# Optimization experiments

Hardware: AMD Instinct MI355X
Metric: run time of the kernel (lower is better)

The kernel has to match this reference:

```python
import jax, jax.numpy as jnp
import numpy as np

HID = 2048
NH = 16
HD = HID // NH  # 128
THETA = 10000.0


def _rope_cos_sin(position_ids):
    # inv_freq: [HD/2]
    inv_freq = 1.0 / (THETA ** (jnp.arange(0, HD, 2, dtype=jnp.float32) / HD))
    freqs = position_ids.astype(jnp.float32)[:, :, None] * inv_freq[None, None, :]  # [b,s,hd/2]
    emb = jnp.concatenate([freqs, freqs], axis=-1)  # [b,s,hd]
    return jnp.cos(emb), jnp.sin(emb)


def _rotate_half(x):
    x1, x2 = x[..., : HD // 2], x[..., HD // 2:]
    return jnp.concatenate([-x2, x1], axis=-1)


def setup_inputs() -> dict:
    key = jax.random.key(0)
    ks = jax.random.split(key, 10)
    b, s = 2, 2048
    scale = 1.0 / np.sqrt(HID)
    hidden_states = jax.random.normal(ks[0], (b, s, HID), dtype=jnp.float32)
    wq = jax.random.normal(ks[1], (HID, HID), dtype=jnp.float32) * scale
    wk = jax.random.normal(ks[2], (HID, HID), dtype=jnp.float32) * scale
    wv = jax.random.normal(ks[3], (HID, HID), dtype=jnp.float32) * scale
    wo = jax.random.normal(ks[4], (HID, HID), dtype=jnp.float32) * scale
    bq = jnp.zeros((HID,), jnp.float32)
    bk = jnp.zeros((HID,), jnp.float32)
    bv = jnp.zeros((HID,), jnp.float32)
    bo = jnp.zeros((HID,), jnp.float32)
    # HF-style additive causal mask [b,1,q,kv]: 0 on/below diag, large negative above
    neg = jnp.finfo(jnp.float32).min
    causal = jnp.where(jnp.tril(jnp.ones((s, s), dtype=bool)), 0.0, neg)
    attention_mask = jnp.broadcast_to(causal[None, None], (b, 1, s, s)).astype(jnp.float32)
    position_ids = jnp.broadcast_to(jnp.arange(s, dtype=jnp.int32)[None], (b, s))
    return {
        "hidden_states": hidden_states,
        "wq": wq, "bq": bq, "wk": wk, "bk": bk,
        "wv": wv, "bv": bv, "wo": wo, "bo": bo,
        "attention_mask": attention_mask, "position_ids": position_ids,
    }


def reference(hidden_states, wq, bq, wk, bk, wv, bv, wo, bo, attention_mask, position_ids):
    b, s, _ = hidden_states.shape
    q = hidden_states @ wq.T + bq  # [b,s,hid]
    k = hidden_states @ wk.T + bk
    v = hidden_states @ wv.T + bv
    # [b, nh, s, hd]
    q = q.reshape(b, s, NH, HD).transpose(0, 2, 1, 3)
    k = k.reshape(b, s, NH, HD).transpose(0, 2, 1, 3)
    v = v.reshape(b, s, NH, HD).transpose(0, 2, 1, 3)
    cos, sin = _rope_cos_sin(position_ids)  # [b,s,hd]
    cos, sin = cos[:, None], sin[:, None]  # unsqueeze_dim=1 -> [b,1,s,hd]
    q = q * cos + _rotate_half(q) * sin
    k = k * cos + _rotate_half(k) * sin
    scores = jnp.einsum("bhqd,bhkd->bhqk", q, k) / np.sqrt(HD)
    scores = scores + attention_mask
    attn = jax.nn.softmax(scores.astype(jnp.float32), axis=-1).astype(q.dtype)
    out = jnp.einsum("bhqk,bhkd->bhqd", attn, v)  # [b,nh,s,hd]
    out = out.transpose(0, 2, 1, 3).reshape(b, s, HID)
    return out @ wo.T + bo
```

## Files before the change

kernel.cpp:

```cpp
#include <hip/hip_runtime.h>

#define S_LEN 2048
#define HID   2048
#define NHEAD 16
#define HDIM  128
#define BATCH 2
#define KDIM  2048

using bf16x8  = __attribute__((ext_vector_type(8))) short;
using f32x4   = __attribute__((ext_vector_type(4))) float;
using f32x16  = __attribute__((ext_vector_type(16))) float;
using short4v = __attribute__((ext_vector_type(4))) short;
using uint4v  = __attribute__((ext_vector_type(4))) unsigned;

__device__ __forceinline__ short f2bf(float f) {
  union { float f; unsigned u; } v; v.f = f;
  unsigned r = v.u + 0x7fffu + ((v.u >> 16) & 1u);
  return (short)(r >> 16);
}
__device__ __forceinline__ float bf2f(short s) {
  union { unsigned u; float f; } v;
  v.u = ((unsigned)(unsigned short)s) << 16;
  return v.f;
}

__device__ __forceinline__ void gl_lds16(const void* g, void* l) {
  __builtin_amdgcn_global_load_lds(
      (const __attribute__((address_space(1))) void*)g,
      (__attribute__((address_space(3))) void*)l, 16, 0, 0);
}

__global__ __launch_bounds__(256)
void convert_all(const float* __restrict__ hs, const float* __restrict__ wq,
                 const float* __restrict__ wk, const float* __restrict__ wv,
                 const float* __restrict__ wo,
                 short* __restrict__ hsb, short* __restrict__ wqkv,
                 short* __restrict__ wob)
{
  const int base = blockIdx.x * 256 + threadIdx.x;
#pragma unroll
  for (int it = 0; it < 6; ++it) {
    int j = base + it * 524288;
    const float* src; short* dst;
    if (j < 1048576)      { src = hs; dst = hsb; }
    else if (j < 1572864) { j -= 1048576; src = wq; dst = wqkv; }
    else if (j < 2097152) { j -= 1572864; src = wk; dst = wqkv + 4194304; }
    else if (j < 2621440) { j -= 2097152; src = wv; dst = wqkv + 8388608; }
    else                  { j -= 2621440; src = wo; dst = wob; }
    f32x4 a = ((const f32x4*)src)[2 * j];
    f32x4 b = ((const f32x4*)src)[2 * j + 1];
    bf16x8 o;
    o[0]=f2bf(a[0]); o[1]=f2bf(a[1]); o[2]=f2bf(a[2]); o[3]=f2bf(a[3]);
    o[4]=f2bf(b[0]); o[5]=f2bf(b[1]); o[6]=f2bf(b[2]); o[7]=f2bf(b[3]);
    ((bf16x8*)dst)[j] = o;
  }
}

template<int KIND>
__global__ __launch_bounds__(256)
void gemm128(const short* __restrict__ A, const short* __restrict__ B,
             const float* __restrict__ bias0, const float* __restrict__ bias1,
             const float* __restrict__ bias2,
             void* __restrict__ O0, void* __restrict__ O1, void* __restrict__ O2)
{
  __shared__ __align__(16) short As[128 * 64];
  __shared__ __align__(16) short Bs[128 * 64];
  const int tid  = threadIdx.x;
  const int lane = tid & 63, wave = tid >> 6;
  const int ln = lane & 15, g = lane >> 4;
  const int wr = wave >> 1, wc = wave & 1;
  const int m0 = blockIdx.x * 128, n0 = blockIdx.y * 128;

  const int srow   = tid >> 3;
  const int schunk = (tid & 7) ^ (srow & 7);
  const short* aS = A + (size_t)(m0 + srow) * KDIM + schunk * 8;
  const short* bS = B + (size_t)(n0 + srow) * KDIM + schunk * 8;

  f32x4 acc[4][4] = {};

  for (int k0 = 0; k0 < KDIM; k0 += 64) {
    __syncthreads();
#pragma unroll
    for (int j = 0; j < 4; ++j) {
      gl_lds16(aS + k0 + j * (32 * KDIM), &As[j * 2048 + tid * 8]);
      gl_lds16(bS + k0 + j * (32 * KDIM), &Bs[j * 2048 + tid * 8]);
    }
    __syncthreads();

#pragma unroll
    for (int ks = 0; ks < 2; ++ks) {
      bf16x8 af[4], bfm[4];
#pragma unroll
      for (int i = 0; i < 4; ++i) {
        const int r = wr * 64 + i * 16 + ln;
        af[i] = *(const bf16x8*)&As[r * 64 + (((ks * 4 + g) ^ (r & 7)) << 3)];
      }
#pragma unroll
      for (int j2 = 0; j2 < 4; ++j2) {
        const int r = wc * 64 + j2 * 16 + ln;
        bfm[j2] = *(const bf16x8*)&Bs[r * 64 + (((ks * 4 + g) ^ (r & 7)) << 3)];
      }
#pragma unroll
      for (int i = 0; i < 4; ++i)
#pragma unroll
        for (int j2 = 0; j2 < 4; ++j2)
          acc[i][j2] = __builtin_amdgcn_mfma_f32_16x16x32_bf16(af[i], bfm[j2], acc[i][j2], 0, 0, 0);
    }
  }

  if constexpr (KIND == 0) {
    const int seg   = n0 >> 11;
    const int nbase = (n0 & 2047) + wc * 64;
    const float* bias = (seg == 0) ? bias0 : (seg == 1) ? bias1 : bias2;
    float bvv[4];
#pragma unroll
    for (int j = 0; j < 4; ++j) bvv[j] = bias[nbase + j * 16 + ln];
    if (seg < 2) {
      short* C = (short*)(seg ? O1 : O0);
#pragma unroll
      for (int i = 0; i < 4; ++i) {
        const int mb = m0 + wr * 64 + i * 16 + 4 * g;
#pragma unroll
        for (int j = 0; j < 4; ++j) {
          const int nl = nbase + j * 16 + ln;
          const int h = nl >> 7, d = nl & 127;
#pragma unroll
          for (int e = 0; e < 4; ++e) {
            const int m = mb + e, bb = m >> 11, t = m & (S_LEN - 1);
            C[((size_t)((bb * NHEAD + h) * S_LEN + t) << 7) + d] = f2bf(acc[i][j][e] + bvv[j]);
          }
        }
      }
    } else {
      short* C = (short*)O2;
#pragma unroll
      for (int i = 0; i < 4; ++i) {
        const int mb = m0 + wr * 64 + i * 16 + 4 * g;
        const int bb = mb >> 11, t0 = mb & (S_LEN - 1);
#pragma unroll
        for (int j = 0; j < 4; ++j) {
          const int nl = nbase + j * 16 + ln;
          const int h = nl >> 7, d = nl & 127;
          short4v v;
#pragma unroll
          for (int e = 0; e < 4; ++e) v[e] = f2bf(acc[i][j][e] + bvv[j]);
          *(short4v*)&C[((size_t)((bb * NHEAD + h) * HDIM + d)) * S_LEN + t0] = v;
        }
      }
    }
  } else {
    float* C = (float*)O0;
    float bvv[4];
#pragma unroll
    for (int j = 0; j < 4; ++j) bvv[j] = bias0[n0 + wc * 64 + j * 16 + ln];
#pragma unroll
    for (int i = 0; i < 4; ++i) {
      const int mb = m0 + wr * 64 + i * 16 + 4 * g;
#pragma unroll
      for (int j = 0; j < 4; ++j) {
        const int n = n0 + wc * 64 + j * 16 + ln;
#pragma unroll
        for (int e = 0; e < 4; ++e)
          C[(size_t)(mb + e) * HID + n] = acc[i][j][e] + bvv[j];
      }
    }
  }
}

#define QSCALE 0.12752767502f
__global__ __launch_bounds__(256)
void rope_kernel(short* __restrict__ Qb, short* __restrict__ Kb,
                 const int* __restrict__ pos_ids)
{
  const int row = blockIdx.x * 4 + (threadIdx.x >> 6);
  const int d   = threadIdx.x & 63;
  const int bh  = row >> 11, t = row & (S_LEN - 1);
  const int b   = bh >> 4;
  const float pos = (float)pos_ids[b * S_LEN + t];
  const float inv = exp2f((float)d * -0.20762050593f);
  float s, c;
  sincosf(pos * inv, &s, &c);
  const size_t base = (size_t)row * HDIM;
  {
    float x1 = bf2f(Qb[base + d]), x2 = bf2f(Qb[base + d + 64]);
    Qb[base + d]      = f2bf((x1 * c - x2 * s) * QSCALE);
    Qb[base + d + 64] = f2bf((x2 * c + x1 * s) * QSCALE);
  }
  {
    float x1 = bf2f(Kb[base + d]), x2 = bf2f(Kb[base + d + 64]);
    Kb[base + d]      = f2bf(x1 * c - x2 * s);
    Kb[base + d + 64] = f2bf(x2 * c + x1 * s);
  }
}

__global__ __launch_bounds__(256)
void attn_kernel(const short* __restrict__ Qb, const short* __restrict__ Kb,
                 const short* __restrict__ Vt, short* __restrict__ AO)
{
  __shared__ __align__(16) short Ks[128 * 128];
  __shared__ __align__(16) short Vs[128 * 128];
  const int tid  = threadIdx.x;
  const int wave = tid >> 6, lane = tid & 63;
  const int lq = lane & 31, lh = lane >> 5;
  const int bid = blockIdx.x;
  const int bh  = bid & 31;
  const int grp = bid >> 5;
  const int yt  = (grp & 7) ^ ((grp & 8) ? 15 : 0);
  const int qw  = yt * 128 + wave * 32;
  const int q   = qw + lq;

  const short* Kbh = Kb + (size_t)bh * (S_LEN * HDIM);
  const short* Vbh = Vt + (size_t)bh * (S_LEN * HDIM);
  const int sw   = ((tid & 15) ^ ((tid >> 4) & 7)) << 3;
  const int kOff = (tid >> 4) * HDIM + sw;
  const int vOff = (tid >> 4) * S_LEN + sw;

  bf16x8 qf[8];
#pragma unroll
  for (int kk = 0; kk < 8; ++kk)
    qf[kk] = *(const bf16x8*)&Qb[((size_t)bh * S_LEN + q) * HDIM + kk * 16 + lh * 8];

  f32x16 o[4] = {};
  float m_s = -3.0e38f, l_s = 0.f;

  for (int kvt = 0; kvt <= yt; ++kvt) {
    const int kv0 = kvt * 128;
    __syncthreads();
#pragma unroll
    for (int p = 0; p < 8; ++p) {
      gl_lds16(Kbh + (size_t)kv0 * HDIM + kOff + p * (16 * HDIM), &Ks[p * 2048 + tid * 8]);
      gl_lds16(Vbh + kv0 + vOff + p * (16 * S_LEN),               &Vs[p * 2048 + tid * 8]);
    }
    __syncthreads();

#pragma unroll
    for (int h = 0; h < 2; ++h) {
      f32x16 sfr[2] = {};
      __builtin_amdgcn_s_setprio(1);
#pragma unroll
      for (int kk = 0; kk < 8; ++kk) {
#pragma unroll
        for (int nt = 0; nt < 2; ++nt) {
          const int row = h * 64 + nt * 32 + lq;
          bf16x8 ak = *(const bf16x8*)&Ks[(row * 128 + kk * 16 + lh * 8) ^ ((row & 7) << 3)];
          sfr[nt] = __builtin_amdgcn_mfma_f32_32x32x16_bf16(ak, qf[kk], sfr[nt], 0, 0, 0);
        }
      }
      __builtin_amdgcn_s_setprio(0);

      if (kvt == yt) {
#pragma unroll
        for (int nt = 0; nt < 2; ++nt) {
          const int kvb = kv0 + h * 64 + nt * 32 + 4 * lh;
#pragma unroll
          for (int r = 0; r < 16; ++r) {
            const int kv = kvb + (r & 3) + 8 * (r >> 2);
            if (kv > q) sfr[nt][r] = -3.0e38f;
          }
        }
      }
      float rmax = -3.0e38f;
#pragma unroll
      for (int nt = 0; nt < 2; ++nt)
#pragma unroll
        for (int r = 0; r < 16; ++r) rmax = fmaxf(rmax, sfr[nt][r]);
      rmax = fmaxf(rmax, __shfl_xor(rmax, 32));

      if (__any(rmax > m_s + 8.0f)) {
        const float nm = fmaxf(m_s, rmax);
        const float corr = exp2f(m_s - nm);
        m_s = nm;
        l_s *= corr;
#pragma unroll
        for (int dt = 0; dt < 4; ++dt)
#pragma unroll
          for (int r = 0; r < 16; ++r) o[dt][r] *= corr;
      }

      float ps = 0.f;
#pragma unroll
      for (int nt = 0; nt < 2; ++nt)
#pragma unroll
        for (int r = 0; r < 16; ++r) {
          const float pv = exp2f(sfr[nt][r] - m_s);
          sfr[nt][r] = pv;
          ps += pv;
        }
      l_s += ps;

      bf16x8 pa[4];
#pragma unroll
      for (int kk = 0; kk < 4; ++kk) {
        const int nt = kk >> 1, c8 = (kk & 1) * 8;
        unsigned w0, w1, w2, w3;
        asm("v_cvt_pk_bf16_f32 %0, %1, %2" : "=v"(w0) : "v"(sfr[nt][c8 + 0]), "v"(sfr[nt][c8 + 1]));
        asm("v_cvt_pk_bf16_f32 %0, %1, %2" : "=v"(w1) : "v"(sfr[nt][c8 + 2]), "v"(sfr[nt][c8 + 3]));
        asm("v_cvt_pk_bf16_f32 %0, %1, %2" : "=v"(w2) : "v"(sfr[nt][c8 + 4]), "v"(sfr[nt][c8 + 5]));
        asm("v_cvt_pk_bf16_f32 %0, %1, %2" : "=v"(w3) : "v"(sfr[nt][c8 + 6]), "v"(sfr[nt][c8 + 7]));
        asm volatile("v_permlane32_swap_b32 %0, %1" : "+v"(w0), "+v"(w2));
        asm volatile("v_permlane32_swap_b32 %0, %1" : "+v"(w1), "+v"(w3));
        uint4v u; u[0] = w0; u[1] = w1; u[2] = w2; u[3] = w3;
        pa[kk] = __builtin_bit_cast(bf16x8, u);
      }

      __builtin_amdgcn_s_setprio(1);
#pragma unroll
      for (int kk = 0; kk < 4; ++kk) {
#pragma unroll
        for (int dt = 0; dt < 4; ++dt) {
          const int row = dt * 32 + lq;
          bf16x8 av = *(const bf16x8*)&Vs[(row * 128 + h * 64 + kk * 16 + lh * 8) ^ ((row & 7) << 3)];
          o[dt] = __builtin_amdgcn_mfma_f32_32x32x16_bf16(av, pa[kk], o[dt], 0, 0, 0);
        }
      }
      __builtin_amdgcn_s_setprio(0);
    }
  }

  l_s += __shfl_xor(l_s, 32);
  const float inv = 1.0f / l_s;
  const int b = bh >> 4, hh = bh & 15;
  short* dst = &AO[((size_t)b * S_LEN + q) * HID + hh * HDIM];
#pragma unroll
  for (int dt = 0; dt < 4; ++dt) {
#pragma unroll
    for (int rq = 0; rq < 4; ++rq) {
      short4v v4;
#pragma unroll
      for (int e = 0; e < 4; ++e) v4[e] = f2bf(o[dt][rq * 4 + e] * inv);
      *(short4v*)&dst[dt * 32 + rq * 8 + 4 * lh] = v4;
    }
  }
}

extern "C" void kernel_launch(void* const* d_in, const int* in_sizes, int n_in,
                              void* d_out, int out_size, void* d_ws, size_t ws_size,
                              hipStream_t stream)
{
  const float* hs = (const float*)d_in[0];
  const float* wq = (const float*)d_in[1];
  const float* bq = (const float*)d_in[2];
  const float* wk = (const float*)d_in[3];
  const float* bk = (const float*)d_in[4];
  const float* wv = (const float*)d_in[5];
  const float* bv = (const float*)d_in[6];
  const float* wo = (const float*)d_in[7];
  const float* bo = (const float*)d_in[8];
  const int*  pos = (const int*)d_in[10];
  float* out = (float*)d_out;

  const size_t TSZ = (size_t)BATCH * NHEAD * S_LEN * HDIM;
  short* Qb   = (short*)d_ws;
  short* Kb   = Qb + TSZ;
  short* Vt   = Kb + TSZ;
  short* hsb  = Vt + TSZ;
  short* AO   = hsb;
  short* Wqkv = hsb + TSZ;
  short* wob  = Wqkv + 12582912;

  convert_all<<<2048, 256, 0, stream>>>(hs, wq, wk, wv, wo, hsb, Wqkv, wob);
  gemm128<0><<<dim3(32, 48), 256, 0, stream>>>(hsb, Wqkv, bq, bk, bv, Qb, Kb, Vt);
  rope_kernel<<<(BATCH * NHEAD * S_LEN) / 4, 256, 0, stream>>>(Qb, Kb, pos);
  attn_kernel<<<512, 256, 0, stream>>>(Qb, Kb, Vt, AO);
  gemm128<1><<<dim3(32, 16), 256, 0, stream>>>(AO, wob, bo, nullptr, nullptr, out, nullptr, nullptr);
}
```

Measured before the change: 254.3 us.

## Use 128x256 GEMM tiles with triple-buffered async LDS pipeline

Replaces the 128x128, 256-thread GEMM with a 128x256 tile computed by 512 threads. K-tiles are triple-buffered in LDS with loads issued two tiles ahead and partial vmcnt waits. Global loads are interleaved between MFMA phases, with setprio raised around the MFMA blocks. The goal is to hide global-to-LDS latency and raise MFMA utilisation in the QKV and output projections. The cost is more LDS per block (about 144KB) and fewer blocks in the grid, which may limit occupancy and wave-level parallelism.

```diff
diff --git a/kernel.cpp b/kernel.cpp
--- a/kernel.cpp
+++ b/kernel.cpp
@@ -57,93 +57,125 @@
 }
 
 template<int KIND>
-__global__ __launch_bounds__(256)
-void gemm128(const short* __restrict__ A, const short* __restrict__ B,
+__global__ __launch_bounds__(512)
+void gemm256(const short* __restrict__ A, const short* __restrict__ B,
              const float* __restrict__ bias0, const float* __restrict__ bias1,
              const float* __restrict__ bias2,
              void* __restrict__ O0, void* __restrict__ O1, void* __restrict__ O2)
 {
-  __shared__ __align__(16) short As[128 * 64];
-  __shared__ __align__(16) short Bs[128 * 64];
+  __shared__ __align__(16) short LA[3 * 8192];
+  __shared__ __align__(16) short LB[3 * 16384];
   const int tid  = threadIdx.x;
   const int lane = tid & 63, wave = tid >> 6;
   const int ln = lane & 15, g = lane >> 4;
-  const int wr = wave >> 1, wc = wave & 1;
-  const int m0 = blockIdx.x * 128, n0 = blockIdx.y * 128;
+  const int wm = wave >> 2, wn = wave & 3;
+  const int m0 = blockIdx.x * 128, n0 = blockIdx.y * 256;
 
   const int srow   = tid >> 3;
   const int schunk = (tid & 7) ^ (srow & 7);
   const short* aS = A + (size_t)(m0 + srow) * KDIM + schunk * 8;
   const short* bS = B + (size_t)(n0 + srow) * KDIM + schunk * 8;
 
+  const int rA = wm * 64 + ln;
+  const int rB = wn * 64 + ln;
+  const int axor = rA & 7, bxor = rB & 7;
+
   f32x4 acc[4][4] = {};
 
-  for (int k0 = 0; k0 < KDIM; k0 += 64) {
-    __syncthreads();
-#pragma unroll
-    for (int j = 0; j < 4; ++j) {
-      gl_lds16(aS + k0 + j * (32 * KDIM), &As[j * 2048 + tid * 8]);
-      gl_lds16(bS + k0 + j * (32 * KDIM), &Bs[j * 2048 + tid * 8]);
-    }
-    __syncthreads();
-
-#pragma unroll
-    for (int ks = 0; ks < 2; ++ks) {
-      bf16x8 af[4], bfm[4];
-#pragma unroll
-      for (int i = 0; i < 4; ++i) {
-        const int r = wr * 64 + i * 16 + ln;
-        af[i] = *(const bf16x8*)&As[r * 64 + (((ks * 4 + g) ^ (r & 7)) << 3)];
-      }
-#pragma unroll
-      for (int j2 = 0; j2 < 4; ++j2) {
-        const int r = wc * 64 + j2 * 16 + ln;
-        bfm[j2] = *(const bf16x8*)&Bs[r * 64 + (((ks * 4 + g) ^ (r & 7)) << 3)];
-      }
-#pragma unroll
-      for (int i = 0; i < 4; ++i)
-#pragma unroll
-        for (int j2 = 0; j2 < 4; ++j2)
-          acc[i][j2] = __builtin_amdgcn_mfma_f32_16x16x32_bf16(af[i], bfm[j2], acc[i][j2], 0, 0, 0);
-    }
-  }
+  auto stA = [&](int T, int b, int j) {
+    gl_lds16(aS + (size_t)(j * 64) * KDIM + T * 64, &LA[b * 8192 + j * 4096 + tid * 8]);
+  };
+  auto stB = [&](int T, int b, int j) {
+    gl_lds16(bS + (size_t)(j * 64) * KDIM + T * 64, &LB[b * 16384 + j * 4096 + tid * 8]);
+  };
+
+  stA(0,0,0); stA(0,0,1); stB(0,0,0); stB(0,0,1); stB(0,0,2); stB(0,0,3);
+  stA(1,1,0); stA(1,1,1); stB(1,1,0); stB(1,1,1); stB(1,1,2); stB(1,1,3);
+
+#define GTILE(T, VMC, DS)                                                      \
+  {                                                                            \
+    if (DS) { stA((T)+2, bs, 0); stA((T)+2, bs, 1); stB((T)+2, bs, 0); }       \
+    asm volatile("s_waitcnt vmcnt(" #VMC ")" ::: "memory");                    \
+    __builtin_amdgcn_s_barrier();                                              \
+    __builtin_amdgcn_sched_barrier(0);                                         \
+    const short* la = &LA[cur * 8192];                                         \
+    const short* lb = &LB[cur * 16384];                                        \
+    bf16x8 bfr[4][2], afr[2][2];                                               \
+    _Pragma("unroll") for (int nf = 0; nf < 4; ++nf)                           \
+      _Pragma("unroll") for (int ks = 0; ks < 2; ++ks)                         \
+        bfr[nf][ks] = *(const bf16x8*)&lb[(rB + nf*16)*64 + (((ks*4+g)^bxor)<<3)]; \
+    _Pragma("unroll") for (int mf = 0; mf < 2; ++mf)                           \
+      _Pragma("unroll") for (int ks = 0; ks < 2; ++ks)                         \
+        afr[mf][ks] = *(const bf16x8*)&la[(rA + mf*16)*64 + (((ks*4+g)^axor)<<3)]; \
+    __builtin_amdgcn_s_setprio(1);                                             \
+    _Pragma("unroll") for (int mf = 0; mf < 2; ++mf)                           \
+      _Pragma("unroll") for (int nf = 0; nf < 4; ++nf)                         \
+        _Pragma("unroll") for (int ks = 0; ks < 2; ++ks)                       \
+          acc[mf][nf] = __builtin_amdgcn_mfma_f32_16x16x32_bf16(               \
+              afr[mf][ks], bfr[nf][ks], acc[mf][nf], 0, 0, 0);                 \
+    __builtin_amdgcn_s_setprio(0);                                             \
+    if (DS) { stB((T)+2, bs, 1); stB((T)+2, bs, 2); stB((T)+2, bs, 3); }       \
+    _Pragma("unroll") for (int mf = 0; mf < 2; ++mf)                           \
+      _Pragma("unroll") for (int ks = 0; ks < 2; ++ks)                         \
+        afr[mf][ks] = *(const bf16x8*)&la[(rA + (mf+2)*16)*64 + (((ks*4+g)^axor)<<3)]; \
+    __builtin_amdgcn_s_setprio(1);                                             \
+    _Pragma("unroll") for (int mf = 0; mf < 2; ++mf)                           \
+      _Pragma("unroll") for (int nf = 0; nf < 4; ++nf)                         \
+        _Pragma("unroll") for (int ks = 0; ks < 2; ++ks)                       \
+          acc[mf+2][nf] = __builtin_amdgcn_mfma_f32_16x16x32_bf16(             \
+              afr[mf][ks], bfr[nf][ks], acc[mf+2][nf], 0, 0, 0);               \
+    __builtin_amdgcn_s_setprio(0);                                             \
+    __builtin_amdgcn_sched_barrier(0);                                         \
+    __builtin_amdgcn_s_barrier();                                              \
+  }
+
+  int cur = 0, bs = 2;
+  for (int T = 0; T < 30; ++T) {
+    GTILE(T, 9, true)
+    cur = (cur == 2) ? 0 : cur + 1;
+    bs  = (bs  == 2) ? 0 : bs  + 1;
+  }
+  GTILE(30, 6, false)
+  cur = (cur == 2) ? 0 : cur + 1;
+  GTILE(31, 0, false)
+#undef GTILE
 
   if constexpr (KIND == 0) {
     const int seg   = n0 >> 11;
-    const int nbase = (n0 & 2047) + wc * 64;
+    const int nbase = (n0 & 2047) + wn * 64;
     const float* bias = (seg == 0) ? bias0 : (seg == 1) ? bias1 : bias2;
     float bvv[4];
 #pragma unroll
-    for (int j = 0; j < 4; ++j) bvv[j] = bias[nbase + j * 16 + ln];
+    for (int nf = 0; nf < 4; ++nf) bvv[nf] = bias[nbase + nf * 16 + ln];
     if (seg < 2) {
       short* C = (short*)(seg ? O1 : O0);
 #pragma unroll
-      for (int i = 0; i < 4; ++i) {
-        const int mb = m0 + wr * 64 + i * 16 + 4 * g;
-#pragma unroll
-        for (int j = 0; j < 4; ++j) {
-          const int nl = nbase + j * 16 + ln;
+      for (int mf = 0; mf < 4; ++mf) {
+        const int mb = m0 + wm * 64 + mf * 16 + 4 * g;
+#pragma unroll
+        for (int nf = 0; nf < 4; ++nf) {
+          const int nl = nbase + nf * 16 + ln;
           const int h = nl >> 7, d = nl & 127;
 #pragma unroll
           for (int e = 0; e < 4; ++e) {
             const int m = mb + e, bb = m >> 11, t = m & (S_LEN - 1);
-            C[((size_t)((bb * NHEAD + h) * S_LEN + t) << 7) + d] = f2bf(acc[i][j][e] + bvv[j]);
+            C[((size_t)((bb * NHEAD + h) * S_LEN + t) << 7) + d] = f2bf(acc[mf][nf][e] + bvv[nf]);
           }
         }
       }
     } else {
       short* C = (short*)O2;
 #pragma unroll
-      for (int i = 0; i < 4; ++i) {
-        const int mb = m0 + wr * 64 + i * 16 + 4 * g;
+      for (int mf = 0; mf < 4; ++mf) {
+        const int mb = m0 + wm * 64 + mf * 16 + 4 * g;
         const int bb = mb >> 11, t0 = mb & (S_LEN - 1);
 #pragma unroll
-        for (int j = 0; j < 4; ++j) {
-          const int nl = nbase + j * 16 + ln;
+        for (int nf = 0; nf < 4; ++nf) {
+          const int nl = nbase + nf * 16 + ln;
           const int h = nl >> 7, d = nl & 127;
           short4v v;
 #pragma unroll
-          for (int e = 0; e < 4; ++e) v[e] = f2bf(acc[i][j][e] + bvv[j]);
+          for (int e = 0; e < 4; ++e) v[e] = f2bf(acc[mf][nf][e] + bvv[nf]);
           *(short4v*)&C[((size_t)((bb * NHEAD + h) * HDIM + d)) * S_LEN + t0] = v;
         }
       }
@@ -152,16 +184,16 @@
     float* C = (float*)O0;
     float bvv[4];
 #pragma unroll
-    for (int j = 0; j < 4; ++j) bvv[j] = bias0[n0 + wc * 64 + j * 16 + ln];
-#pragma unroll
-    for (int i = 0; i < 4; ++i) {
-      const int mb = m0 + wr * 64 + i * 16 + 4 * g;
-#pragma unroll
-      for (int j = 0; j < 4; ++j) {
-        const int n = n0 + wc * 64 + j * 16 + ln;
+    for (int nf = 0; nf < 4; ++nf) bvv[nf] = bias0[n0 + wn * 64 + nf * 16 + ln];
+#pragma unroll
+    for (int mf = 0; mf < 4; ++mf) {
+      const int mb = m0 + wm * 64 + mf * 16 + 4 * g;
+#pragma unroll
+      for (int nf = 0; nf < 4; ++nf) {
+        const int n = n0 + wn * 64 + nf * 16 + ln;
 #pragma unroll
         for (int e = 0; e < 4; ++e)
-          C[(size_t)(mb + e) * HID + n] = acc[i][j][e] + bvv[j];
+          C[(size_t)(mb + e) * HID + n] = acc[mf][nf][e] + bvv[nf];
       }
     }
   }
@@ -359,8 +391,8 @@
   short* wob  = Wqkv + 12582912;
 
   convert_all<<<2048, 256, 0, stream>>>(hs, wq, wk, wv, wo, hsb, Wqkv, wob);
-  gemm128<0><<<dim3(32, 48), 256, 0, stream>>>(hsb, Wqkv, bq, bk, bv, Qb, Kb, Vt);
+  gemm256<0><<<dim3(32, 24), 512, 0, stream>>>(hsb, Wqkv, bq, bk, bv, Qb, Kb, Vt);
   rope_kernel<<<(BATCH * NHEAD * S_LEN) / 4, 256, 0, stream>>>(Qb, Kb, pos);
   attn_kernel<<<512, 256, 0, stream>>>(Qb, Kb, Vt, AO);
-  gemm128<1><<<dim3(32, 16), 256, 0, stream>>>(AO, wob, bo, nullptr, nullptr, out, nullptr, nullptr);
-}
+  gemm256<1><<<dim3(32, 8), 512, 0, stream>>>(AO, wob, bo, nullptr, nullptr, out, nullptr, nullptr);
+}
```

Result: slower. 272.1 us (+7.0%).
